# Kernel optimization log

Hardware: AMD Instinct MI355X
Metric: run time of the kernel (lower is better)

Reference implementation:

```python
import jax, jax.numpy as jnp
import numpy as np

NUM_HEADS = 32
KV_HEADS = 8
HEAD_DIM = 128
HIDDEN = 4096
Q_DIM = NUM_HEADS * HEAD_DIM      # 4096
KV_DIM = KV_HEADS * HEAD_DIM      # 1024
GROUP = NUM_HEADS // KV_HEADS     # 4 (GQA)
ROPE_THETA = 10000.0
LORA_SCALE = 0.5
BP, S = 4, 1024                   # prefill requests x prefill seq len
BD, L = 64, 2048                  # decode requests x cached kv len
R, NA = 16, 8                     # lora rank, num adapters


def _rope(x, pos):
    # x: [..., n_heads, HEAD_DIM]; pos broadcastable over the token dims of x
    half = x.shape[-1] // 2
    inv = 1.0 / (ROPE_THETA ** (jnp.arange(half, dtype=jnp.float32) / half))
    freqs = pos[..., None].astype(jnp.float32) * inv          # pos.shape + (half,)
    cos = jnp.cos(freqs)[..., None, :]                        # insert head axis
    sin = jnp.sin(freqs)[..., None, :]
    x1, x2 = x[..., :half], x[..., half:]
    return jnp.concatenate([x1 * cos - x2 * sin, x2 * cos + x1 * sin], axis=-1)


def _lora(x, A, B, idx):
    # grouped multi-adapter LoRA: per-request adapter selection
    # x: [b, ..., H]; A: [NA, H, R]; B: [NA, R, D]; idx: [b]
    t = jnp.einsum('b...h,bhr->b...r', x, A[idx])
    return LORA_SCALE * jnp.einsum('b...r,brd->b...d', t, B[idx])


def setup_inputs() -> dict:
    key = jax.random.key(0)
    ks = jax.random.split(key, 16)
    T = BP * S + BD
    w = lambda k, shp: (jax.random.normal(k, shp, jnp.float32) * 0.02)
    return {
        'hidden_states': jax.random.normal(ks[0], (T, HIDDEN), jnp.float32),
        'w_qkv': w(ks[1], (HIDDEN, Q_DIM + 2 * KV_DIM)),
        'w_o': w(ks[2], (Q_DIM, HIDDEN)),
        'k_cache': jax.random.normal(ks[3], (BD, L, KV_HEADS, HEAD_DIM), jnp.float32),
        'v_cache': jax.random.normal(ks[4], (BD, L, KV_HEADS, HEAD_DIM), jnp.float32),
        'lora_a_q': w(ks[5], (NA, HIDDEN, R)),
        'lora_b_q': w(ks[6], (NA, R, Q_DIM)),
        'lora_a_k': w(ks[7], (NA, HIDDEN, R)),
        'lora_b_k': w(ks[8], (NA, R, KV_DIM)),
        'lora_a_v': w(ks[9], (NA, HIDDEN, R)),
        'lora_b_v': w(ks[10], (NA, R, KV_DIM)),
        'lora_a_o': w(ks[11], (NA, Q_DIM, R)),
        'lora_b_o': w(ks[12], (NA, R, HIDDEN)),
        'prefill_adapter_idx': jax.random.randint(ks[13], (BP,), 0, NA),
        'decode_adapter_idx': jax.random.randint(ks[14], (BD,), 0, NA),
    }


def reference(hidden_states, w_qkv, w_o, k_cache, v_cache,
              lora_a_q, lora_b_q, lora_a_k, lora_b_k, lora_a_v, lora_b_v,
              lora_a_o, lora_b_o, prefill_adapter_idx, decode_adapter_idx):
    TP = BP * S
    qkv = hidden_states @ w_qkv
    q, k, v = jnp.split(qkv, [Q_DIM, Q_DIM + KV_DIM], axis=1)

    x_p = hidden_states[:TP].reshape(BP, S, HIDDEN)
    x_d = hidden_states[TP:]

    # apply_lora_weight_kvq: per-request adapters on q/k/v
    q_p = q[:TP].reshape(BP, S, Q_DIM) + _lora(x_p, lora_a_q, lora_b_q, prefill_adapter_idx)
    k_p = k[:TP].reshape(BP, S, KV_DIM) + _lora(x_p, lora_a_k, lora_b_k, prefill_adapter_idx)
    v_p = v[:TP].reshape(BP, S, KV_DIM) + _lora(x_p, lora_a_v, lora_b_v, prefill_adapter_idx)
    q_d = q[TP:] + _lora(x_d, lora_a_q, lora_b_q, decode_adapter_idx)
    k_d = k[TP:] + _lora(x_d, lora_a_k, lora_b_k, decode_adapter_idx)
    v_d = v[TP:] + _lora(x_d, lora_a_v, lora_b_v, decode_adapter_idx)

    scale = 1.0 / np.sqrt(HEAD_DIM).astype(np.float32)

    # ---- prefill: causal self-attention with on-the-fly RoPE ----
    q_p = _rope(q_p.reshape(BP, S, NUM_HEADS, HEAD_DIM), jnp.arange(S, dtype=jnp.float32))
    k_p = _rope(k_p.reshape(BP, S, KV_HEADS, HEAD_DIM), jnp.arange(S, dtype=jnp.float32))
    v_p = v_p.reshape(BP, S, KV_HEADS, HEAD_DIM)
    kr = jnp.repeat(k_p, GROUP, axis=2)
    vr = jnp.repeat(v_p, GROUP, axis=2)
    scores = jnp.einsum('bqhd,bkhd->bhqk', q_p, kr) * scale
    causal = jnp.tril(jnp.ones((S, S), bool))
    scores = jnp.where(causal, scores, -jnp.inf)
    attn = jax.nn.softmax(scores, axis=-1)
    out_p = jnp.einsum('bhqk,bkhd->bqhd', attn, vr).reshape(TP, Q_DIM)

    # ---- decode: one new token per request vs paged KV cache ----
    q_d = _rope(q_d.reshape(BD, NUM_HEADS, HEAD_DIM), jnp.asarray(L, jnp.float32))
    k_new = _rope(k_d.reshape(BD, KV_HEADS, HEAD_DIM), jnp.asarray(L, jnp.float32))
    k_hist = _rope(k_cache, jnp.arange(L, dtype=jnp.float32))
    k_all = jnp.concatenate([k_hist, k_new[:, None]], axis=1)   # [BD, L+1, kvh, hd]
    v_all = jnp.concatenate([v_cache, v_d.reshape(BD, 1, KV_HEADS, HEAD_DIM)], axis=1)
    kr2 = jnp.repeat(k_all, GROUP, axis=2)
    vr2 = jnp.repeat(v_all, GROUP, axis=2)
    s2 = jnp.einsum('bhd,bkhd->bhk', q_d, kr2) * scale
    a2 = jax.nn.softmax(s2, axis=-1)
    out_d = jnp.einsum('bhk,bkhd->bhd', a2, vr2).reshape(BD, Q_DIM)

    # ---- o_proj + apply_lora_weight_attn ----
    attn_raw = jnp.concatenate([out_p, out_d], axis=0)
    o = attn_raw @ w_o
    o_p = o[:TP].reshape(BP, S, HIDDEN) + _lora(attn_raw[:TP].reshape(BP, S, Q_DIM), lora_a_o, lora_b_o, prefill_adapter_idx)
    o_d = o[TP:] + _lora(attn_raw[TP:], lora_a_o, lora_b_o, decode_adapter_idx)
    return jnp.concatenate([o_p.reshape(TP, HIDDEN), o_d], axis=0)
```

## Files before the change

kernel.cpp:

```cpp
#include <hip/hip_runtime.h>

#define NUM_HEADS 32
#define KV_HEADS 8
#define HEAD_DIM 128
#define HIDDEN 4096
#define Q_DIM 4096
#define KV_DIM 1024
#define QKV_DIM 6144
#define GROUP 4
#define BP 4
#define S_LEN 1024
#define BD 64
#define L_CTX 2048
#define RANK 16
#define NA 8
#define TP (BP * S_LEN)
#define T_TOT (TP + BD)
#define M_PAD 4224
#define SCALE 0.08838834764831845f
#define LORA_SCALE 0.5f
#define DNSPLIT 16
#define DSPLIT_LEN 128
#define DP_STRIDE 520

typedef float fv4 __attribute__((ext_vector_type(4)));
typedef __bf16 bf16x8 __attribute__((ext_vector_type(8)));
typedef unsigned short usv4 __attribute__((ext_vector_type(4)));
typedef unsigned short u16;

__device__ __forceinline__ float b2f(u16 u) {
    unsigned int x = ((unsigned int)u) << 16;
    return __builtin_bit_cast(float, x);
}
__device__ __forceinline__ u16 f2b(float f) {
    unsigned int u = __builtin_bit_cast(unsigned int, f);
    unsigned int r = u + 0x7fffu + ((u >> 16) & 1u);
    return (u16)(r >> 16);
}
__device__ __forceinline__ void gload_lds16(const void* g, void* l) {
    __builtin_amdgcn_global_load_lds((const __attribute__((address_space(1))) void*)g,
                                     (__attribute__((address_space(3))) void*)l, 16, 0, 0);
}

#define OFF_QKV  ((size_t)0)
#define OFF_ATTN OFF_QKV
#define OFF_HB   ((size_t)51904512)
#define OFF_QP   OFF_HB
#define OFF_WOT  OFF_HB
#define OFF_WQT  ((size_t)86507520)
#define OFF_KP   ((size_t)86507520)
#define OFF_VP   ((size_t)94896128)
#define OFF_QD   ((size_t)103284736)
#define OFF_KD   ((size_t)104333312)
#define OFF_VD   ((size_t)104595456)
#define OFF_DP   ((size_t)104857600)
#define OFF_T    ((size_t)136839168)
#define OFF_TO   ((size_t)137637888)
#define OFF_COS  ((size_t)137904128)
#define OFF_SIN  ((size_t)138428672)

__global__ void rope_tab_kernel(float* ctab, float* stab) {
    int idx = blockIdx.x * 256 + threadIdx.x;
    if (idx >= 2049 * 64) return;
    int pos = idx >> 6, d = idx & 63;
    float inv = 1.0f / powf(10000.0f, (float)d / 64.0f);
    float f = (float)pos * inv;
    ctab[idx] = cosf(f);
    stab[idx] = sinf(f);
}

__global__ void conv_hidden_kernel(const float* __restrict__ x, u16* __restrict__ y) {
    int gid = blockIdx.x * 256 + threadIdx.x;
    if (gid >= M_PAD * (HIDDEN / 8)) return;
    size_t base = (size_t)gid * 8;
    int row = gid >> 9;
    usv4 lo, hi;
    if (row < T_TOT) {
        fv4 a = *(const fv4*)(x + base);
        fv4 b = *(const fv4*)(x + base + 4);
        lo[0] = f2b(a[0]); lo[1] = f2b(a[1]); lo[2] = f2b(a[2]); lo[3] = f2b(a[3]);
        hi[0] = f2b(b[0]); hi[1] = f2b(b[1]); hi[2] = f2b(b[2]); hi[3] = f2b(b[3]);
    } else {
        lo[0] = 0; lo[1] = 0; lo[2] = 0; lo[3] = 0;
        hi[0] = 0; hi[1] = 0; hi[2] = 0; hi[3] = 0;
    }
    *(usv4*)(y + base) = lo;
    *(usv4*)(y + base + 4) = hi;
}

__global__ __launch_bounds__(256) void transpose_f32_bf16_kernel(const float* __restrict__ in,
                                                                 u16* __restrict__ out,
                                                                 int R, int C) {
    __shared__ float tile[64][65];
    int r0 = blockIdx.y * 64, c0 = blockIdx.x * 64;
    int t = threadIdx.x;
    int tr = t >> 4, tc4 = (t & 15) * 4;
#pragma unroll
    for (int it = 0; it < 4; ++it) {
        int r = tr + it * 16;
        fv4 v = *(const fv4*)(in + (size_t)(r0 + r) * C + c0 + tc4);
        tile[r][tc4 + 0] = v[0]; tile[r][tc4 + 1] = v[1];
        tile[r][tc4 + 2] = v[2]; tile[r][tc4 + 3] = v[3];
    }
    __syncthreads();
#pragma unroll
    for (int it = 0; it < 4; ++it) {
        int c = tr + it * 16;
        usv4 st;
        st[0] = f2b(tile[tc4 + 0][c]); st[1] = f2b(tile[tc4 + 1][c]);
        st[2] = f2b(tile[tc4 + 2][c]); st[3] = f2b(tile[tc4 + 3][c]);
        *(usv4*)(out + (size_t)(c0 + c) * R + r0 + tc4) = st;
    }
}

__global__ __launch_bounds__(256) void lora_a_kernel(const float* __restrict__ x,
                              const float* __restrict__ Aq, const float* __restrict__ Ak,
                              const float* __restrict__ Av,
                              const int* __restrict__ pidx, const int* __restrict__ didx,
                              float* __restrict__ T) {
    __shared__ float xs[4][HIDDEN];
    int t0 = blockIdx.x * 4;
    int tid = threadIdx.x;
    for (int j = tid; j < 4096; j += 256) {
        int tok = j >> 10, off = (j & 1023) * 4;
        *(fv4*)&xs[tok][off] = *(const fv4*)(x + (size_t)(t0 + tok) * HIDDEN + off);
    }
    __syncthreads();
    int w = tid >> 6, lane = tid & 63;
    if (w >= 3) return;
    const float* Ab = (w == 0) ? Aq : (w == 1 ? Ak : Av);
    float acc[4][16];
#pragma unroll
    for (int tk = 0; tk < 4; ++tk)
#pragma unroll
        for (int r = 0; r < 16; ++r) acc[tk][r] = 0.f;
#pragma unroll
    for (int tk = 0; tk < 4; ++tk) {
        int t = t0 + tk;
        int a = (t < TP) ? pidx[t >> 10] : didx[t - TP];
        const float* A = Ab + (size_t)a * HIDDEN * RANK;
        for (int i = 0; i < 64; ++i) {
            int hh = i * 64 + lane;
            float xv = xs[tk][hh];
            const float* Ar = A + (size_t)hh * RANK;
            fv4 a0 = *(const fv4*)Ar, a1 = *(const fv4*)(Ar + 4);
            fv4 a2 = *(const fv4*)(Ar + 8), a3 = *(const fv4*)(Ar + 12);
#pragma unroll
            for (int r = 0; r < 4; ++r) {
                acc[tk][r] += xv * a0[r];
                acc[tk][4 + r] += xv * a1[r];
                acc[tk][8 + r] += xv * a2[r];
                acc[tk][12 + r] += xv * a3[r];
            }
        }
    }
#pragma unroll
    for (int tk = 0; tk < 4; ++tk)
#pragma unroll
        for (int r = 0; r < 16; ++r) {
            float v = acc[tk][r];
            v += __shfl_xor(v, 1); v += __shfl_xor(v, 2); v += __shfl_xor(v, 4);
            v += __shfl_xor(v, 8); v += __shfl_xor(v, 16); v += __shfl_xor(v, 32);
            if (lane == r) T[(size_t)(t0 + tk) * 48 + w * 16 + r] = v;
        }
}

template <int OUT_BF16>
__global__ __launch_bounds__(256) void gemm_bt_kernel(const u16* __restrict__ A,
                                                      const u16* __restrict__ BT,
                                                      void* __restrict__ Cp,
                                                      int Mstore, int N, int K) {
    __shared__ __align__(16) u16 As[2][128 * 32];
    __shared__ __align__(16) u16 Bs[2][128 * 32];
    int tid = threadIdx.x;
    int m0 = blockIdx.y * 128, n0 = blockIdx.x * 128;
    int lane = tid & 63, w = tid >> 6, lr = lane & 15, lg = lane >> 4;
    int wr = w >> 1, wc = w & 1;
    int arow = tid >> 2, acol = (tid & 3) * 8;
    const u16* Ab = A + (size_t)(m0 + arow) * K + acol;
    const u16* Bb = BT + (size_t)(n0 + arow) * K + acol;
    fv4 acc[4][4] = {};
    int nt = K / 32;
#define GSTAGE(buf, kk)                                                             \
    {                                                                               \
        char* Ad = (char*)&As[buf][0] + w * 1024;                                   \
        char* Bd = (char*)&Bs[buf][0] + w * 1024;                                   \
        gload_lds16(Ab + (kk), Ad);                                                 \
        gload_lds16(Ab + (size_t)64 * K + (kk), Ad + 4096);                         \
        gload_lds16(Bb + (kk), Bd);                                                 \
        gload_lds16(Bb + (size_t)64 * K + (kk), Bd + 4096);                         \
    }
    GSTAGE(0, 0)
    __syncthreads();
    int cur = 0;
    for (int t = 0; t < nt; ++t) {
        if (t + 1 < nt) GSTAGE(cur ^ 1, (t + 1) * 32)
        bf16x8 af[4], bf[4];
#pragma unroll
        for (int i = 0; i < 4; ++i) {
            af[i] = *(const bf16x8*)&As[cur][(wr * 64 + i * 16 + lr) * 32 + lg * 8];
            bf[i] = *(const bf16x8*)&Bs[cur][(wc * 64 + i * 16 + lr) * 32 + lg * 8];
        }
#pragma unroll
        for (int mi = 0; mi < 4; ++mi)
#pragma unroll
            for (int ni = 0; ni < 4; ++ni)
                acc[mi][ni] = __builtin_amdgcn_mfma_f32_16x16x32_bf16(af[mi], bf[ni], acc[mi][ni], 0, 0, 0);
        __syncthreads();
        cur ^= 1;
    }
#undef GSTAGE
#pragma unroll
    for (int mi = 0; mi < 4; ++mi)
#pragma unroll
        for (int ni = 0; ni < 4; ++ni) {
            int col = n0 + wc * 64 + ni * 16 + lr;
#pragma unroll
            for (int r = 0; r < 4; ++r) {
                int row = m0 + wr * 64 + mi * 16 + lg * 4 + r;
                if (row < Mstore) {
                    if (OUT_BF16)
                        ((u16*)Cp)[(size_t)row * N + col] = f2b(acc[mi][ni][r]);
                    else
                        ((float*)Cp)[(size_t)row * N + col] = acc[mi][ni][r];
                }
            }
        }
}

__global__ __launch_bounds__(256) void lorab_rope_scatter_kernel(
    const u16* __restrict__ qkv, const float* __restrict__ T,
    const float* __restrict__ Bq, const float* __restrict__ Bk, const float* __restrict__ Bv,
    const int* __restrict__ pidx, const int* __restrict__ didx,
    const float* __restrict__ ctab, const float* __restrict__ stab,
    u16* __restrict__ qp, u16* __restrict__ kp, u16* __restrict__ vp,
    float* __restrict__ qd, float* __restrict__ kd, float* __restrict__ vd) {
    int t = blockIdx.x;
    __shared__ float Ts[48];
    if (threadIdx.x < 48) Ts[threadIdx.x] = T[(size_t)t * 48 + threadIdx.x];
    __syncthreads();
    bool pre = t < TP;
    int a = pre ? pidx[t >> 10] : didx[t - TP];
    int pos = pre ? (t & 1023) : L_CTX;
    int b = t >> 10;
    int td = t - TP;
    const u16* qrow = qkv + (size_t)t * QKV_DIM;
    for (int p = threadIdx.x; p < 3072; p += 256) {
        if (p < 2048) {
            int h = p >> 6, d = p & 63;
            int col = h * 128 + d;
            float v1 = b2f(qrow[col]), v2 = b2f(qrow[col + 64]);
            const float* B = Bq + (size_t)a * RANK * Q_DIM;
            float l1 = 0.f, l2 = 0.f;
#pragma unroll
            for (int r = 0; r < 16; ++r) {
                float tv = Ts[r];
                l1 += tv * B[(size_t)r * Q_DIM + col];
                l2 += tv * B[(size_t)r * Q_DIM + col + 64];
            }
            v1 += LORA_SCALE * l1; v2 += LORA_SCALE * l2;
            float c = ctab[pos * 64 + d], s = stab[pos * 64 + d];
            float o1 = v1 * c - v2 * s, o2 = v2 * c + v1 * s;
            if (pre) {
                size_t base = (((size_t)(b * 32 + h)) * 1024 + pos) * 128 + d;
                qp[base] = f2b(o1); qp[base + 64] = f2b(o2);
            } else {
                size_t base = ((size_t)(td * 32 + h)) * 128 + d;
                qd[base] = o1; qd[base + 64] = o2;
            }
        } else if (p < 2560) {
            int pp = p - 2048;
            int h = pp >> 6, d = pp & 63;
            int jc = h * 128 + d;
            int col = Q_DIM + jc;
            float v1 = b2f(qrow[col]), v2 = b2f(qrow[col + 64]);
            const float* B = Bk + (size_t)a * RANK * KV_DIM;
            float l1 = 0.f, l2 = 0.f;
#pragma unroll
            for (int r = 0; r < 16; ++r) {
                float tv = Ts[16 + r];
                l1 += tv * B[(size_t)r * KV_DIM + jc];
                l2 += tv * B[(size_t)r * KV_DIM + jc + 64];
            }
            v1 += LORA_SCALE * l1; v2 += LORA_SCALE * l2;
            float c = ctab[pos * 64 + d], s = stab[pos * 64 + d];
            float o1 = v1 * c - v2 * s, o2 = v2 * c + v1 * s;
            if (pre) {
                size_t base = (((size_t)(b * 8 + h)) * 1024 + pos) * 128 + d;
                kp[base] = f2b(o1); kp[base + 64] = f2b(o2);
            } else {
                size_t base = ((size_t)(td * 8 + h)) * 128 + d;
                kd[base] = o1; kd[base + 64] = o2;
            }
        } else {
            int pp = p - 2560;
            int h = pp >> 6, d = pp & 63;
            int jc = h * 128 + d;
            int col = Q_DIM + KV_DIM + jc;
            float v1 = b2f(qrow[col]), v2 = b2f(qrow[col + 64]);
            const float* B = Bv + (size_t)a * RANK * KV_DIM;
            float l1 = 0.f, l2 = 0.f;
#pragma unroll
            for (int r = 0; r < 16; ++r) {
                float tv = Ts[32 + r];
                l1 += tv * B[(size_t)r * KV_DIM + jc];
                l2 += tv * B[(size_t)r * KV_DIM + jc + 64];
            }
            v1 += LORA_SCALE * l1; v2 += LORA_SCALE * l2;
            if (pre) {
                size_t base = (((size_t)(b * 8 + h)) * 1024 + pos) * 128 + d;
                vp[base] = f2b(v1); vp[base + 64] = f2b(v2);
            } else {
                size_t base = ((size_t)(td * 8 + h)) * 128 + d;
                vd[base] = v1; vd[base + 64] = v2;
            }
        }
    }
}

__global__ __launch_bounds__(256) void prefill_attn_kernel(const u16* __restrict__ qp,
                                                           const u16* __restrict__ kp,
                                                           const u16* __restrict__ vp,
                                                           u16* __restrict__ attn) {
    int bx = blockIdx.x;
    int qt = (bx & 1) ? (31 - (bx >> 1)) : (bx >> 1);
    int kvh = blockIdx.y, b = blockIdx.z;
    int tid = threadIdx.x, w = tid >> 6, lane = tid & 63, lr = lane & 15, lg = lane >> 4;
    int h = kvh * 4 + w;
    const u16* Q = qp + ((size_t)(b * 32 + h)) * 1024 * 128;
    const u16* K = kp + ((size_t)(b * 8 + kvh)) * 1024 * 128;
    const u16* V = vp + ((size_t)(b * 8 + kvh)) * 1024 * 128;
    int qc0 = qt * 32 + lr, qc1 = qt * 32 + 16 + lr;
    bf16x8 qf0[4], qf1[4];
#pragma unroll
    for (int dc = 0; dc < 4; ++dc) {
        qf0[dc] = *(const bf16x8*)(Q + (size_t)qc0 * 128 + dc * 32 + lg * 8);
        qf1[dc] = *(const bf16x8*)(Q + (size_t)qc1 * 128 + dc * 32 + lg * 8);
    }
    fv4 o0[8] = {}, o1[8] = {};
    float m0 = -INFINITY, l0 = 0.f;
    float m1 = -INFINITY, l1 = 0.f;
    int nkb = qt + 1;
    for (int kb = 0; kb < nkb; ++kb) {
        int k0 = kb * 32;
        fv4 s00 = {}, s10 = {}, s01 = {}, s11 = {};
#pragma unroll
        for (int dc = 0; dc < 4; ++dc) {
            bf16x8 kf0 = *(const bf16x8*)(K + (size_t)(k0 + lr) * 128 + dc * 32 + lg * 8);
            bf16x8 kf1 = *(const bf16x8*)(K + (size_t)(k0 + 16 + lr) * 128 + dc * 32 + lg * 8);
            s00 = __builtin_amdgcn_mfma_f32_16x16x32_bf16(kf0, qf0[dc], s00, 0, 0, 0);
            s10 = __builtin_amdgcn_mfma_f32_16x16x32_bf16(kf1, qf0[dc], s10, 0, 0, 0);
            s01 = __builtin_amdgcn_mfma_f32_16x16x32_bf16(kf0, qf1[dc], s01, 0, 0, 0);
            s11 = __builtin_amdgcn_mfma_f32_16x16x32_bf16(kf1, qf1[dc], s11, 0, 0, 0);
        }
        bf16x8 vf[8];
#pragma unroll
        for (int c = 0; c < 8; ++c)
#pragma unroll
            for (int i = 0; i < 4; ++i) {
                vf[c][i] = __builtin_bit_cast(__bf16, V[(size_t)(k0 + lg * 4 + i) * 128 + c * 16 + lr]);
                vf[c][4 + i] = __builtin_bit_cast(__bf16, V[(size_t)(k0 + 16 + lg * 4 + i) * 128 + c * 16 + lr]);
            }
        bf16x8 pf0, pf1;
        {
            float p0[4], p1[4];
            float lm = -INFINITY;
#pragma unroll
            for (int r = 0; r < 4; ++r) {
                float x = s00[r] * SCALE;
                if (k0 + lg * 4 + r > qc0) x = -INFINITY;
                p0[r] = x; lm = fmaxf(lm, x);
                x = s10[r] * SCALE;
                if (k0 + 16 + lg * 4 + r > qc0) x = -INFINITY;
                p1[r] = x; lm = fmaxf(lm, x);
            }
            lm = fmaxf(lm, __shfl_xor(lm, 16));
            lm = fmaxf(lm, __shfl_xor(lm, 32));
            float mn = fmaxf(m0, lm);
            float sc = __expf(m0 - mn);
            float rs = 0.f;
#pragma unroll
            for (int r = 0; r < 4; ++r) {
                p0[r] = __expf(p0[r] - mn);
                p1[r] = __expf(p1[r] - mn);
                rs += p0[r] + p1[r];
            }
            rs += __shfl_xor(rs, 16);
            rs += __shfl_xor(rs, 32);
            l0 = l0 * sc + rs;
            m0 = mn;
#pragma unroll
            for (int c = 0; c < 8; ++c) o0[c] *= sc;
#pragma unroll
            for (int r = 0; r < 4; ++r) {
                pf0[r] = (__bf16)p0[r];
                pf0[4 + r] = (__bf16)p1[r];
            }
        }
        {
            float p0[4], p1[4];
            float lm = -INFINITY;
#pragma unroll
            for (int r = 0; r < 4; ++r) {
                float x = s01[r] * SCALE;
                if (k0 + lg * 4 + r > qc1) x = -INFINITY;
                p0[r] = x; lm = fmaxf(lm, x);
                x = s11[r] * SCALE;
                if (k0 + 16 + lg * 4 + r > qc1) x = -INFINITY;
                p1[r] = x; lm = fmaxf(lm, x);
            }
            lm = fmaxf(lm, __shfl_xor(lm, 16));
            lm = fmaxf(lm, __shfl_xor(lm, 32));
            float mn = fmaxf(m1, lm);
            float sc = __expf(m1 - mn);
            float rs = 0.f;
#pragma unroll
            for (int r = 0; r < 4; ++r) {
                p0[r] = __expf(p0[r] - mn);
                p1[r] = __expf(p1[r] - mn);
                rs += p0[r] + p1[r];
            }
            rs += __shfl_xor(rs, 16);
            rs += __shfl_xor(rs, 32);
            l1 = l1 * sc + rs;
            m1 = mn;
#pragma unroll
            for (int c = 0; c < 8; ++c) o1[c] *= sc;
#pragma unroll
            for (int r = 0; r < 4; ++r) {
                pf1[r] = (__bf16)p0[r];
                pf1[4 + r] = (__bf16)p1[r];
            }
        }
#pragma unroll
        for (int c = 0; c < 8; ++c) {
            o0[c] = __builtin_amdgcn_mfma_f32_16x16x32_bf16(vf[c], pf0, o0[c], 0, 0, 0);
            o1[c] = __builtin_amdgcn_mfma_f32_16x16x32_bf16(vf[c], pf1, o1[c], 0, 0, 0);
        }
    }
    float inv0 = 1.0f / l0, inv1 = 1.0f / l1;
    size_t trow0 = (size_t)(b * 1024 + qc0) * Q_DIM;
    size_t trow1 = (size_t)(b * 1024 + qc1) * Q_DIM;
#pragma unroll
    for (int c = 0; c < 8; ++c)
#pragma unroll
        for (int r = 0; r < 4; ++r) {
            int feat = h * 128 + c * 16 + lg * 4 + r;
            attn[trow0 + feat] = f2b(o0[c][r] * inv0);
            attn[trow1 + feat] = f2b(o1[c][r] * inv1);
        }
}

template <int FIRST_HALF>
__device__ __forceinline__ bf16x8 krope8(const float* __restrict__ Krow,
                                         const float* __restrict__ ct,
                                         const float* __restrict__ st, int d0) {
    bf16x8 out;
    if (FIRST_HALF) {
        fv4 a0 = *(const fv4*)(Krow + d0), a1 = *(const fv4*)(Krow + d0 + 4);
        fv4 b0 = *(const fv4*)(Krow + d0 + 64), b1 = *(const fv4*)(Krow + d0 + 68);
        fv4 c0 = *(const fv4*)(ct + d0), c1 = *(const fv4*)(ct + d0 + 4);
        fv4 s0 = *(const fv4*)(st + d0), s1 = *(const fv4*)(st + d0 + 4);
#pragma unroll
        for (int i = 0; i < 4; ++i) {
            out[i] = (__bf16)(a0[i] * c0[i] - b0[i] * s0[i]);
            out[4 + i] = (__bf16)(a1[i] * c1[i] - b1[i] * s1[i]);
        }
    } else {
        int dd = d0 - 64;
        fv4 a0 = *(const fv4*)(Krow + d0), a1 = *(const fv4*)(Krow + d0 + 4);
        fv4 b0 = *(const fv4*)(Krow + dd), b1 = *(const fv4*)(Krow + dd + 4);
        fv4 c0 = *(const fv4*)(ct + dd), c1 = *(const fv4*)(ct + dd + 4);
        fv4 s0 = *(const fv4*)(st + dd), s1 = *(const fv4*)(st + dd + 4);
#pragma unroll
        for (int i = 0; i < 4; ++i) {
            out[i] = (__bf16)(a0[i] * c0[i] + b0[i] * s0[i]);
            out[4 + i] = (__bf16)(a1[i] * c1[i] + b1[i] * s1[i]);
        }
    }
    return out;
}

__global__ __launch_bounds__(128) void decode_attn_kernel(const float* __restrict__ kc,
                                                          const float* __restrict__ vc,
                                                          const float* __restrict__ qd,
                                                          const float* __restrict__ ctab,
                                                          const float* __restrict__ stab,
                                                          float* __restrict__ dp) {
    int blk = blockIdx.x;
    int bk = blk >> 3;
    int b = bk >> 3, kvh = bk & 7;
    int wv = threadIdx.x >> 6, lane = threadIdx.x & 63;
    int s = (blk & 7) * 2 + wv;
    int lr = lane & 15, lg = lane >> 4;
    const float* Qrow = qd + ((size_t)(b * 32 + kvh * 4 + (lr & 3))) * 128;
    bf16x8 qf[4];
#pragma unroll
    for (int dc = 0; dc < 4; ++dc) {
        int d0 = dc * 32 + lg * 8;
        fv4 q0 = *(const fv4*)(Qrow + d0), q1 = *(const fv4*)(Qrow + d0 + 4);
#pragma unroll
        for (int i = 0; i < 4; ++i) {
            qf[dc][i] = (__bf16)q0[i];
            qf[dc][4 + i] = (__bf16)q1[i];
        }
    }
    fv4 o[8] = {};
    float m = -INFINITY, l = 0.f;
    int kbase = s * DSPLIT_LEN;
    for (int t = 0; t < 4; ++t) {
        int k0 = kbase + t * 32;
        int key0 = k0 + lr, key1 = k0 + 16 + lr;
        const float* K0 = kc + (((size_t)b * L_CTX + key0) * 8 + kvh) * 128;
        const float* K1 = kc + (((size_t)b * L_CTX + key1) * 8 + kvh) * 128;
        const float* ct0 = ctab + key0 * 64;
        const float* st0 = stab + key0 * 64;
        const float* ct1 = ctab + key1 * 64;
        const float* st1 = stab + key1 * 64;
        fv4 s0 = {}, s1 = {};
#pragma unroll
        for (int dc = 0; dc < 4; ++dc) {
            int d0 = dc * 32 + lg * 8;
            bf16x8 kf0, kf1;
            if (dc < 2) {
                kf0 = krope8<1>(K0, ct0, st0, d0);
                kf1 = krope8<1>(K1, ct1, st1, d0);
            } else {
                kf0 = krope8<0>(K0, ct0, st0, d0);
                kf1 = krope8<0>(K1, ct1, st1, d0);
            }
            s0 = __builtin_amdgcn_mfma_f32_16x16x32_bf16(kf0, qf[dc], s0, 0, 0, 0);
            s1 = __builtin_amdgcn_mfma_f32_16x16x32_bf16(kf1, qf[dc], s1, 0, 0, 0);
        }
        const float* Vb = vc + (((size_t)b * L_CTX + k0) * 8 + kvh) * 128;
        bf16x8 vf[8];
#pragma unroll
        for (int c = 0; c < 8; ++c)
#pragma unroll
            for (int i = 0; i < 4; ++i) {
                vf[c][i] = (__bf16)Vb[(size_t)(lg * 4 + i) * 1024 + c * 16 + lr];
                vf[c][4 + i] = (__bf16)Vb[(size_t)(16 + lg * 4 + i) * 1024 + c * 16 + lr];
            }
        float p0[4], p1[4];
        float lm = -INFINITY;
#pragma unroll
        for (int r = 0; r < 4; ++r) {
            float x = s0[r] * SCALE;
            p0[r] = x; lm = fmaxf(lm, x);
            x = s1[r] * SCALE;
            p1[r] = x; lm = fmaxf(lm, x);
        }
        lm = fmaxf(lm, __shfl_xor(lm, 16));
        lm = fmaxf(lm, __shfl_xor(lm, 32));
        float mn = fmaxf(m, lm);
        float sc = __expf(m - mn);
        float rs = 0.f;
#pragma unroll
        for (int r = 0; r < 4; ++r) {
            p0[r] = __expf(p0[r] - mn);
            p1[r] = __expf(p1[r] - mn);
            rs += p0[r] + p1[r];
        }
        rs += __shfl_xor(rs, 16);
        rs += __shfl_xor(rs, 32);
        l = l * sc + rs;
        m = mn;
#pragma unroll
        for (int c = 0; c < 8; ++c) o[c] *= sc;
        bf16x8 pf;
#pragma unroll
        for (int r = 0; r < 4; ++r) {
            pf[r] = (__bf16)p0[r];
            pf[4 + r] = (__bf16)p1[r];
        }
#pragma unroll
        for (int c = 0; c < 8; ++c)
            o[c] = __builtin_amdgcn_mfma_f32_16x16x32_bf16(vf[c], pf, o[c], 0, 0, 0);
    }
    size_t base = ((size_t)(bk * DNSPLIT + s)) * DP_STRIDE;
    if (lr < 4) {
#pragma unroll
        for (int c = 0; c < 8; ++c)
#pragma unroll
            for (int r = 0; r < 4; ++r)
                dp[base + 8 + lr * 128 + c * 16 + lg * 4 + r] = o[c][r];
        if (lg == 0) { dp[base + lr] = m; dp[base + 4 + lr] = l; }
    }
}

__global__ __launch_bounds__(256) void decode_merge_kernel(const float* __restrict__ dp,
                                                           const float* __restrict__ qd,
                                                           const float* __restrict__ kd,
                                                           const float* __restrict__ vd,
                                                           u16* __restrict__ attn) {
    int bk = blockIdx.x;
    int b = bk >> 3, kvh = bk & 7;
    int g = threadIdx.x >> 6, lane = threadIdx.x & 63;
    size_t qb = ((size_t)(b * 32 + kvh * 4 + g)) * 128;
    float q1 = qd[qb + lane], q2 = qd[qb + 64 + lane];
    size_t kb = ((size_t)(b * 8 + kvh)) * 128;
    float k1 = kd[kb + lane], k2 = kd[kb + 64 + lane];
    float v1 = vd[kb + lane], v2 = vd[kb + 64 + lane];
    float part = q1 * k1 + q2 * k2;
#pragma unroll
    for (int off = 32; off; off >>= 1) part += __shfl_xor(part, off);
    float snew = part * SCALE;
    float M = snew;
#pragma unroll
    for (int s = 0; s < DNSPLIT; ++s)
        M = fmaxf(M, dp[((size_t)(bk * DNSPLIT + s)) * DP_STRIDE + g]);
    float L = 0.f, O1 = 0.f, O2 = 0.f;
#pragma unroll
    for (int s = 0; s < DNSPLIT; ++s) {
        size_t base = ((size_t)(bk * DNSPLIT + s)) * DP_STRIDE;
        float e = __expf(dp[base + g] - M);
        L += dp[base + 4 + g] * e;
        O1 += dp[base + 8 + g * 128 + lane] * e;
        O2 += dp[base + 8 + g * 128 + 64 + lane] * e;
    }
    float en = __expf(snew - M);
    L += en; O1 += en * v1; O2 += en * v2;
    size_t orow = (size_t)(TP + b) * Q_DIM + (kvh * 4 + g) * 128;
    attn[orow + lane] = f2b(O1 / L);
    attn[orow + 64 + lane] = f2b(O2 / L);
}

__global__ __launch_bounds__(64) void lora_o_a_kernel(const u16* __restrict__ attn,
                                const float* __restrict__ Ao,
                                const int* __restrict__ pidx, const int* __restrict__ didx,
                                float* __restrict__ To) {
    __shared__ float xs[4][HIDDEN];
    int t0 = blockIdx.x * 4;
    int lane = threadIdx.x;
    for (int j = lane; j < 4096; j += 64) {
        int tok = j >> 10, off = (j & 1023) * 4;
        usv4 v = *(const usv4*)(attn + (size_t)(t0 + tok) * Q_DIM + off);
        xs[tok][off] = b2f(v[0]); xs[tok][off + 1] = b2f(v[1]);
        xs[tok][off + 2] = b2f(v[2]); xs[tok][off + 3] = b2f(v[3]);
    }
    __syncthreads();
    float acc[4][16];
#pragma unroll
    for (int tk = 0; tk < 4; ++tk)
#pragma unroll
        for (int r = 0; r < 16; ++r) acc[tk][r] = 0.f;
#pragma unroll
    for (int tk = 0; tk < 4; ++tk) {
        int t = t0 + tk;
        int a = (t < TP) ? pidx[t >> 10] : didx[t - TP];
        const float* A = Ao + (size_t)a * Q_DIM * RANK;
        for (int i = 0; i < 64; ++i) {
            int hh = i * 64 + lane;
            float xv = xs[tk][hh];
            const float* Ar = A + (size_t)hh * RANK;
            fv4 a0 = *(const fv4*)Ar, a1 = *(const fv4*)(Ar + 4);
            fv4 a2 = *(const fv4*)(Ar + 8), a3 = *(const fv4*)(Ar + 12);
#pragma unroll
            for (int r = 0; r < 4; ++r) {
                acc[tk][r] += xv * a0[r];
                acc[tk][4 + r] += xv * a1[r];
                acc[tk][8 + r] += xv * a2[r];
                acc[tk][12 + r] += xv * a3[r];
            }
        }
    }
#pragma unroll
    for (int tk = 0; tk < 4; ++tk)
#pragma unroll
        for (int r = 0; r < 16; ++r) {
            float v = acc[tk][r];
            v += __shfl_xor(v, 1); v += __shfl_xor(v, 2); v += __shfl_xor(v, 4);
            v += __shfl_xor(v, 8); v += __shfl_xor(v, 16); v += __shfl_xor(v, 32);
            if (lane == r) To[(size_t)(t0 + tk) * RANK + r] = v;
        }
}

__global__ void final_lora_add_kernel(float* __restrict__ out, const float* __restrict__ To,
                                      const float* __restrict__ Bo,
                                      const int* __restrict__ pidx, const int* __restrict__ didx) {
    int gid = blockIdx.x * 256 + threadIdx.x;
    if (gid >= T_TOT * HIDDEN) return;
    int t = gid >> 12, j = gid & 4095;
    int a = (t < TP) ? pidx[t >> 10] : didx[t - TP];
    const float* B = Bo + (size_t)a * RANK * HIDDEN;
    const float* Tr = To + (size_t)t * RANK;
    float acc = 0.f;
#pragma unroll
    for (int r = 0; r < 16; ++r) acc += Tr[r] * B[(size_t)r * HIDDEN + j];
    out[gid] += LORA_SCALE * acc;
}

extern "C" void kernel_launch(void* const* d_in, const int* in_sizes, int n_in,
                              void* d_out, int out_size, void* d_ws, size_t ws_size,
                              hipStream_t stream) {
    const float* hidden = (const float*)d_in[0];
    const float* w_qkv = (const float*)d_in[1];
    const float* w_o = (const float*)d_in[2];
    const float* k_cache = (const float*)d_in[3];
    const float* v_cache = (const float*)d_in[4];
    const float* Aq = (const float*)d_in[5];
    const float* Bq = (const float*)d_in[6];
    const float* Ak = (const float*)d_in[7];
    const float* Bk = (const float*)d_in[8];
    const float* Av = (const float*)d_in[9];
    const float* Bv = (const float*)d_in[10];
    const float* Ao = (const float*)d_in[11];
    const float* Bo = (const float*)d_in[12];
    const int* pidx = (const int*)d_in[13];
    const int* didx = (const int*)d_in[14];
    float* out = (float*)d_out;

    char* ws = (char*)d_ws;
    u16* qkv = (u16*)(ws + OFF_QKV);
    u16* attn = (u16*)(ws + OFF_ATTN);
    u16* hb = (u16*)(ws + OFF_HB);
    u16* wqT = (u16*)(ws + OFF_WQT);
    u16* woT = (u16*)(ws + OFF_WOT);
    float* T = (float*)(ws + OFF_T);
    u16* qp = (u16*)(ws + OFF_QP);
    u16* kp = (u16*)(ws + OFF_KP);
    u16* vp = (u16*)(ws + OFF_VP);
    float* qd = (float*)(ws + OFF_QD);
    float* kd = (float*)(ws + OFF_KD);
    float* vd = (float*)(ws + OFF_VD);
    float* dp = (float*)(ws + OFF_DP);
    float* To = (float*)(ws + OFF_TO);
    float* ctab = (float*)(ws + OFF_COS);
    float* stab = (float*)(ws + OFF_SIN);

    rope_tab_kernel<<<513, 256, 0, stream>>>(ctab, stab);
    conv_hidden_kernel<<<(M_PAD * (HIDDEN / 8) + 255) / 256, 256, 0, stream>>>(hidden, hb);
    transpose_f32_bf16_kernel<<<dim3(QKV_DIM / 64, HIDDEN / 64), 256, 0, stream>>>(w_qkv, wqT, HIDDEN, QKV_DIM);
    lora_a_kernel<<<T_TOT / 4, 256, 0, stream>>>(hidden, Aq, Ak, Av, pidx, didx, T);
    gemm_bt_kernel<1><<<dim3(QKV_DIM / 128, M_PAD / 128), 256, 0, stream>>>(hb, wqT, qkv, M_PAD, QKV_DIM, HIDDEN);
    lorab_rope_scatter_kernel<<<T_TOT, 256, 0, stream>>>(qkv, T, Bq, Bk, Bv, pidx, didx,
                                                         ctab, stab, qp, kp, vp, qd, kd, vd);
    prefill_attn_kernel<<<dim3(32, 8, 4), 256, 0, stream>>>(qp, kp, vp, attn);
    decode_attn_kernel<<<4096, 128, 0, stream>>>(k_cache, v_cache, qd, ctab, stab, dp);
    decode_merge_kernel<<<512, 256, 0, stream>>>(dp, qd, kd, vd, attn);
    transpose_f32_bf16_kernel<<<dim3(HIDDEN / 64, Q_DIM / 64), 256, 0, stream>>>(w_o, woT, Q_DIM, HIDDEN);
    lora_o_a_kernel<<<T_TOT / 4, 64, 0, stream>>>(attn, Ao, pidx, didx, To);
    gemm_bt_kernel<0><<<dim3(HIDDEN / 128, M_PAD / 128), 256, 0, stream>>>(attn, woT, out, T_TOT, HIDDEN, Q_DIM);
    final_lora_add_kernel<<<(T_TOT * HIDDEN + 255) / 256, 256, 0, stream>>>(out, To, Bo, pidx, didx);
}
```

Baseline: 1.589 ms.

## Replace GEMM with 256x256-tile 8-wave kernel with interleaved loads and swizzled LDS

The 128x128, 4-wave bf16 GEMM is replaced by a 256x256-tile, 8-wave kernel with a K-step of 64. Each iteration is split into four MFMA phases, and the next tile's global-to-LDS loads are interleaved between them using explicit barriers, waitcnts and setprio. An XOR swizzle on LDS columns is meant to avoid bank conflicts, and the larger tile raises data reuse per loaded byte. The trade-off is a 17x24 or 17x16 grid that only partly covers the padded M, heavier LDS use, more registers and a fragile hand-written sync schedule.

```diff
diff --git a/kernel.cpp b/kernel.cpp
--- a/kernel.cpp
+++ b/kernel.cpp
@@ -165,64 +165,131 @@
         }
 }
 
+#define MFMA16(d, a, b_) d = __builtin_amdgcn_mfma_f32_16x16x32_bf16(a, b_, d, 0, 0, 0)
 template <int OUT_BF16>
-__global__ __launch_bounds__(256) void gemm_bt_kernel(const u16* __restrict__ A,
-                                                      const u16* __restrict__ BT,
-                                                      void* __restrict__ Cp,
-                                                      int Mstore, int N, int K) {
-    __shared__ __align__(16) u16 As[2][128 * 32];
-    __shared__ __align__(16) u16 Bs[2][128 * 32];
+__global__ __launch_bounds__(512) void gemm8_kernel(const u16* __restrict__ A,
+                                                    const u16* __restrict__ BT,
+                                                    void* __restrict__ Cp,
+                                                    int Mstore, int N, int K) {
+    __shared__ __align__(16) u16 As[2][16384];
+    __shared__ __align__(16) u16 Bs[2][16384];
     int tid = threadIdx.x;
-    int m0 = blockIdx.y * 128, n0 = blockIdx.x * 128;
-    int lane = tid & 63, w = tid >> 6, lr = lane & 15, lg = lane >> 4;
-    int wr = w >> 1, wc = w & 1;
-    int arow = tid >> 2, acol = (tid & 3) * 8;
-    const u16* Ab = A + (size_t)(m0 + arow) * K + acol;
-    const u16* Bb = BT + (size_t)(n0 + arow) * K + acol;
-    fv4 acc[4][4] = {};
-    int nt = K / 32;
-#define GSTAGE(buf, kk)                                                             \
-    {                                                                               \
-        char* Ad = (char*)&As[buf][0] + w * 1024;                                   \
-        char* Bd = (char*)&Bs[buf][0] + w * 1024;                                   \
-        gload_lds16(Ab + (kk), Ad);                                                 \
-        gload_lds16(Ab + (size_t)64 * K + (kk), Ad + 4096);                         \
-        gload_lds16(Bb + (kk), Bd);                                                 \
-        gload_lds16(Bb + (size_t)64 * K + (kk), Bd + 4096);                         \
-    }
-    GSTAGE(0, 0)
-    __syncthreads();
-    int cur = 0;
-    for (int t = 0; t < nt; ++t) {
-        if (t + 1 < nt) GSTAGE(cur ^ 1, (t + 1) * 32)
-        bf16x8 af[4], bf[4];
-#pragma unroll
-        for (int i = 0; i < 4; ++i) {
-            af[i] = *(const bf16x8*)&As[cur][(wr * 64 + i * 16 + lr) * 32 + lg * 8];
-            bf[i] = *(const bf16x8*)&Bs[cur][(wc * 64 + i * 16 + lr) * 32 + lg * 8];
-        }
-#pragma unroll
-        for (int mi = 0; mi < 4; ++mi)
-#pragma unroll
-            for (int ni = 0; ni < 4; ++ni)
-                acc[mi][ni] = __builtin_amdgcn_mfma_f32_16x16x32_bf16(af[mi], bf[ni], acc[mi][ni], 0, 0, 0);
-        __syncthreads();
-        cur ^= 1;
-    }
-#undef GSTAGE
-#pragma unroll
-    for (int mi = 0; mi < 4; ++mi)
-#pragma unroll
-        for (int ni = 0; ni < 4; ++ni) {
-            int col = n0 + wc * 64 + ni * 16 + lr;
+    int m0 = blockIdx.y * 256, n0 = blockIdx.x * 256;
+    int w = tid >> 6, lane = tid & 63, lr = lane & 15, lg = lane >> 4;
+    int wm = w >> 2, wn = w & 3;
+    int tswz = tid ^ (((tid >> 5) & 1) << 1);
+    int rbase = tswz >> 3, cbase = (tswz & 7) * 8;
+    const u16* Ag = A + (size_t)m0 * K;
+    const u16* Bg = BT + (size_t)n0 * K;
+    int xr16 = (lr & 4) << 2;
+    int cs0 = (lg * 8) ^ xr16;
+    int cs1 = (32 + lg * 8) ^ xr16;
+    int arow = wm * 128 + lr;
+    int brow = wn * 64 + lr;
+    fv4 acc[8][4] = {};
+    int nt = K / 64;
+#define STG(Xg, hh, kk, tile)                                                          \
+    {                                                                                  \
+        gload_lds16((Xg) + (size_t)((hh)*128 + rbase) * K + (kk) + cbase,              \
+                    (void*)(&(tile)[(hh)*8192 + w * 512]));                            \
+        gload_lds16((Xg) + (size_t)((hh)*128 + 64 + rbase) * K + (kk) + cbase,         \
+                    (void*)(&(tile)[(hh)*8192 + 4096 + w * 512]));                     \
+    }
+    STG(Bg, 0, 0, Bs[0]) STG(Ag, 0, 0, As[0]) STG(Ag, 1, 0, As[0]) STG(Bg, 1, 0, Bs[0])
+    STG(Bg, 0, 64, Bs[1]) STG(Ag, 0, 64, As[1]) STG(Ag, 1, 64, As[1])
+    asm volatile("s_waitcnt vmcnt(6)" ::: "memory");
+    __builtin_amdgcn_s_barrier();
+    for (int T = 0; T < nt; ++T) {
+        int b = T & 1;
+        int k0 = T * 64;
+        const u16* At = &As[b][0];
+        const u16* Bt = &Bs[b][0];
+        bf16x8 aR[4][2], a2R[4][2], bR[4][2];
+#pragma unroll
+        for (int mf = 0; mf < 4; ++mf) {
+            int r = (arow + mf * 16) * 64;
+            aR[mf][0] = *(const bf16x8*)(At + r + cs0);
+            aR[mf][1] = *(const bf16x8*)(At + r + cs1);
+        }
+#pragma unroll
+        for (int nf = 0; nf < 4; ++nf) {
+            int r = (brow + nf * 16) * 64;
+            bR[nf][0] = *(const bf16x8*)(Bt + r + cs0);
+            bR[nf][1] = *(const bf16x8*)(Bt + r + cs1);
+        }
+        if (T + 1 < nt) STG(Bg, 1, k0 + 64, Bs[b ^ 1])
+        __builtin_amdgcn_s_barrier();
+        asm volatile("s_waitcnt lgkmcnt(0)" ::: "memory");
+        __builtin_amdgcn_s_setprio(1);
+#pragma unroll
+        for (int mf = 0; mf < 4; ++mf)
+#pragma unroll
+            for (int nf = 0; nf < 2; ++nf) {
+                MFMA16(acc[mf][nf], aR[mf][0], bR[nf][0]);
+                MFMA16(acc[mf][nf], aR[mf][1], bR[nf][1]);
+            }
+        __builtin_amdgcn_s_setprio(0);
+        __builtin_amdgcn_s_barrier();
+#pragma unroll
+        for (int mf = 0; mf < 4; ++mf) {
+            int r = (arow + 64 + mf * 16) * 64;
+            a2R[mf][0] = *(const bf16x8*)(At + r + cs0);
+            a2R[mf][1] = *(const bf16x8*)(At + r + cs1);
+        }
+        if (T + 2 < nt) STG(Bg, 0, k0 + 128, Bs[b])
+        __builtin_amdgcn_s_barrier();
+        asm volatile("s_waitcnt lgkmcnt(0)" ::: "memory");
+        __builtin_amdgcn_s_setprio(1);
+#pragma unroll
+        for (int mf = 0; mf < 4; ++mf)
+#pragma unroll
+            for (int nf = 0; nf < 2; ++nf) {
+                MFMA16(acc[mf][2 + nf], aR[mf][0], bR[2 + nf][0]);
+                MFMA16(acc[mf][2 + nf], aR[mf][1], bR[2 + nf][1]);
+            }
+        __builtin_amdgcn_s_setprio(0);
+        __builtin_amdgcn_s_barrier();
+        if (T + 2 < nt) STG(Ag, 0, k0 + 128, As[b])
+        __builtin_amdgcn_s_barrier();
+        asm volatile("s_waitcnt lgkmcnt(0)" ::: "memory");
+        __builtin_amdgcn_s_setprio(1);
+#pragma unroll
+        for (int mf = 0; mf < 4; ++mf)
+#pragma unroll
+            for (int nf = 0; nf < 2; ++nf) {
+                MFMA16(acc[4 + mf][nf], a2R[mf][0], bR[nf][0]);
+                MFMA16(acc[4 + mf][nf], a2R[mf][1], bR[nf][1]);
+            }
+        __builtin_amdgcn_s_setprio(0);
+        __builtin_amdgcn_s_barrier();
+        if (T + 2 < nt) STG(Ag, 1, k0 + 128, As[b])
+        asm volatile("s_waitcnt vmcnt(6)" ::: "memory");
+        __builtin_amdgcn_s_barrier();
+        __builtin_amdgcn_s_setprio(1);
+#pragma unroll
+        for (int mf = 0; mf < 4; ++mf)
+#pragma unroll
+            for (int nf = 0; nf < 2; ++nf) {
+                MFMA16(acc[4 + mf][2 + nf], a2R[mf][0], bR[2 + nf][0]);
+                MFMA16(acc[4 + mf][2 + nf], a2R[mf][1], bR[2 + nf][1]);
+            }
+        __builtin_amdgcn_s_setprio(0);
+        __builtin_amdgcn_s_barrier();
+    }
+#undef STG
+#pragma unroll
+    for (int mf = 0; mf < 8; ++mf)
+#pragma unroll
+        for (int nf = 0; nf < 4; ++nf) {
+            int col = n0 + wn * 64 + nf * 16 + lr;
 #pragma unroll
             for (int r = 0; r < 4; ++r) {
-                int row = m0 + wr * 64 + mi * 16 + lg * 4 + r;
+                int row = m0 + wm * 128 + mf * 16 + lg * 4 + r;
                 if (row < Mstore) {
                     if (OUT_BF16)
-                        ((u16*)Cp)[(size_t)row * N + col] = f2b(acc[mi][ni][r]);
+                        ((u16*)Cp)[(size_t)row * N + col] = f2b(acc[mf][nf][r]);
                     else
-                        ((float*)Cp)[(size_t)row * N + col] = acc[mi][ni][r];
+                        ((float*)Cp)[(size_t)row * N + col] = acc[mf][nf][r];
                 }
             }
         }
@@ -732,7 +799,7 @@
     conv_hidden_kernel<<<(M_PAD * (HIDDEN / 8) + 255) / 256, 256, 0, stream>>>(hidden, hb);
     transpose_f32_bf16_kernel<<<dim3(QKV_DIM / 64, HIDDEN / 64), 256, 0, stream>>>(w_qkv, wqT, HIDDEN, QKV_DIM);
     lora_a_kernel<<<T_TOT / 4, 256, 0, stream>>>(hidden, Aq, Ak, Av, pidx, didx, T);
-    gemm_bt_kernel<1><<<dim3(QKV_DIM / 128, M_PAD / 128), 256, 0, stream>>>(hb, wqT, qkv, M_PAD, QKV_DIM, HIDDEN);
+    gemm8_kernel<1><<<dim3(QKV_DIM / 256, 17), 512, 0, stream>>>(hb, wqT, qkv, T_TOT, QKV_DIM, HIDDEN);
     lorab_rope_scatter_kernel<<<T_TOT, 256, 0, stream>>>(qkv, T, Bq, Bk, Bv, pidx, didx,
                                                          ctab, stab, qp, kp, vp, qd, kd, vd);
     prefill_attn_kernel<<<dim3(32, 8, 4), 256, 0, stream>>>(qp, kp, vp, attn);
@@ -740,6 +807,6 @@
     decode_merge_kernel<<<512, 256, 0, stream>>>(dp, qd, kd, vd, attn);
     transpose_f32_bf16_kernel<<<dim3(HIDDEN / 64, Q_DIM / 64), 256, 0, stream>>>(w_o, woT, Q_DIM, HIDDEN);
     lora_o_a_kernel<<<T_TOT / 4, 64, 0, stream>>>(attn, Ao, pidx, didx, To);
-    gemm_bt_kernel<0><<<dim3(HIDDEN / 128, M_PAD / 128), 256, 0, stream>>>(attn, woT, out, T_TOT, HIDDEN, Q_DIM);
+    gemm8_kernel<0><<<dim3(HIDDEN / 256, 17), 512, 0, stream>>>(attn, woT, out, T_TOT, HIDDEN, Q_DIM);
     final_lora_add_kernel<<<(T_TOT * HIDDEN + 255) / 256, 256, 0, stream>>>(out, To, Bo, pidx, didx);
 }
```

Result: slower. 1.655 ms (+4.2%).

## Fuse output LoRA-B add into o_proj GEMM epilogue and swizzle block order

Applied to the files above, without the earlier changes.

The standalone final_lora_add kernel is removed and its rank-16 LoRA-B contribution is computed in the epilogue of the o_proj GEMM, before the output is stored. This saves one full read-modify-write pass over the fp32 output and one kernel launch. Both GEMMs also switch to a 1D grid with an XCD-style block swizzle, which is meant to improve L2 locality across compute dies. The cost is that every output element in the epilogue now does 16 strided Bo loads plus loads of To.

```diff
diff --git a/kernel.cpp b/kernel.cpp
--- a/kernel.cpp
+++ b/kernel.cpp
@@ -165,15 +165,21 @@
         }
 }
 
-template <int OUT_BF16>
+template <int OUT_BF16, int FUSE_LORA>
 __global__ __launch_bounds__(256) void gemm_bt_kernel(const u16* __restrict__ A,
                                                       const u16* __restrict__ BT,
                                                       void* __restrict__ Cp,
-                                                      int Mstore, int N, int K) {
+                                                      int Mstore, int N, int K, int nbx,
+                                                      const float* __restrict__ To,
+                                                      const float* __restrict__ Bo,
+                                                      const int* __restrict__ pidx,
+                                                      const int* __restrict__ didx) {
     __shared__ __align__(16) u16 As[2][128 * 32];
     __shared__ __align__(16) u16 Bs[2][128 * 32];
     int tid = threadIdx.x;
-    int m0 = blockIdx.y * 128, n0 = blockIdx.x * 128;
+    int nwg = gridDim.x, bid = blockIdx.x;
+    int swz = (bid & 7) * (nwg >> 3) + (bid >> 3);
+    int m0 = (swz / nbx) * 128, n0 = (swz % nbx) * 128;
     int lane = tid & 63, w = tid >> 6, lr = lane & 15, lg = lane >> 4;
     int wr = w >> 1, wc = w & 1;
     int arow = tid >> 2, acol = (tid & 3) * 8;
@@ -219,10 +225,21 @@
             for (int r = 0; r < 4; ++r) {
                 int row = m0 + wr * 64 + mi * 16 + lg * 4 + r;
                 if (row < Mstore) {
+                    float val = acc[mi][ni][r];
+                    if (FUSE_LORA) {
+                        int a = (row < TP) ? pidx[row >> 10] : didx[row - TP];
+                        const float* Bo_a = Bo + (size_t)a * RANK * HIDDEN + col;
+                        const float* Tr = To + (size_t)row * RANK;
+                        float s = 0.f;
+#pragma unroll
+                        for (int rr = 0; rr < 16; ++rr)
+                            s += Tr[rr] * Bo_a[(size_t)rr * HIDDEN];
+                        val += LORA_SCALE * s;
+                    }
                     if (OUT_BF16)
-                        ((u16*)Cp)[(size_t)row * N + col] = f2b(acc[mi][ni][r]);
+                        ((u16*)Cp)[(size_t)row * N + col] = f2b(val);
                     else
-                        ((float*)Cp)[(size_t)row * N + col] = acc[mi][ni][r];
+                        ((float*)Cp)[(size_t)row * N + col] = val;
                 }
             }
         }
@@ -675,21 +692,6 @@
         }
 }
 
-__global__ void final_lora_add_kernel(float* __restrict__ out, const float* __restrict__ To,
-                                      const float* __restrict__ Bo,
-                                      const int* __restrict__ pidx, const int* __restrict__ didx) {
-    int gid = blockIdx.x * 256 + threadIdx.x;
-    if (gid >= T_TOT * HIDDEN) return;
-    int t = gid >> 12, j = gid & 4095;
-    int a = (t < TP) ? pidx[t >> 10] : didx[t - TP];
-    const float* B = Bo + (size_t)a * RANK * HIDDEN;
-    const float* Tr = To + (size_t)t * RANK;
-    float acc = 0.f;
-#pragma unroll
-    for (int r = 0; r < 16; ++r) acc += Tr[r] * B[(size_t)r * HIDDEN + j];
-    out[gid] += LORA_SCALE * acc;
-}
-
 extern "C" void kernel_launch(void* const* d_in, const int* in_sizes, int n_in,
                               void* d_out, int out_size, void* d_ws, size_t ws_size,
                               hipStream_t stream) {
@@ -732,7 +734,8 @@
     conv_hidden_kernel<<<(M_PAD * (HIDDEN / 8) + 255) / 256, 256, 0, stream>>>(hidden, hb);
     transpose_f32_bf16_kernel<<<dim3(QKV_DIM / 64, HIDDEN / 64), 256, 0, stream>>>(w_qkv, wqT, HIDDEN, QKV_DIM);
     lora_a_kernel<<<T_TOT / 4, 256, 0, stream>>>(hidden, Aq, Ak, Av, pidx, didx, T);
-    gemm_bt_kernel<1><<<dim3(QKV_DIM / 128, M_PAD / 128), 256, 0, stream>>>(hb, wqT, qkv, M_PAD, QKV_DIM, HIDDEN);
+    gemm_bt_kernel<1, 0><<<(QKV_DIM / 128) * (M_PAD / 128), 256, 0, stream>>>(
+        hb, wqT, qkv, M_PAD, QKV_DIM, HIDDEN, QKV_DIM / 128, nullptr, nullptr, pidx, didx);
     lorab_rope_scatter_kernel<<<T_TOT, 256, 0, stream>>>(qkv, T, Bq, Bk, Bv, pidx, didx,
                                                          ctab, stab, qp, kp, vp, qd, kd, vd);
     prefill_attn_kernel<<<dim3(32, 8, 4), 256, 0, stream>>>(qp, kp, vp, attn);
@@ -740,6 +743,6 @@
     decode_merge_kernel<<<512, 256, 0, stream>>>(dp, qd, kd, vd, attn);
     transpose_f32_bf16_kernel<<<dim3(HIDDEN / 64, Q_DIM / 64), 256, 0, stream>>>(w_o, woT, Q_DIM, HIDDEN);
     lora_o_a_kernel<<<T_TOT / 4, 64, 0, stream>>>(attn, Ao, pidx, didx, To);
-    gemm_bt_kernel<0><<<dim3(HIDDEN / 128, M_PAD / 128), 256, 0, stream>>>(attn, woT, out, T_TOT, HIDDEN, Q_DIM);
-    final_lora_add_kernel<<<(T_TOT * HIDDEN + 255) / 256, 256, 0, stream>>>(out, To, Bo, pidx, didx);
-}
+    gemm_bt_kernel<0, 1><<<(HIDDEN / 128) * (M_PAD / 128), 256, 0, stream>>>(
+        attn, woT, out, T_TOT, HIDDEN, Q_DIM, HIDDEN / 128, To, Bo, pidx, didx);
+}
```

Result: slower. 1.629 ms (+2.6%).
